# Kernel tuning notes

Hardware: AMD Instinct MI355X
Metric: run time of the kernel (lower is better)

Reference implementation:

```python
import jax, jax.numpy as jnp
import numpy as np

N_NODES, N_EDGES, HIDDEN, N_GRAPHS = 100000, 500000, 128, 2048
ATOM_DIM, BOND_DIM, OUT_DIM = 4, 3, 1


def setup_inputs() -> dict:
    key = jax.random.key(0)
    ks = jax.random.split(key, 13)
    s = 0.05  # small init scale to keep relu+scatter depth iterations numerically tame
    return {
        "x": jax.random.normal(ks[0], (N_NODES, ATOM_DIM), jnp.float32),
        "edge_index": jax.random.randint(ks[1], (2, N_EDGES), 0, N_NODES, dtype=jnp.int32),
        "edge_attr": jax.random.normal(ks[2], (N_EDGES, BOND_DIM), jnp.float32),
        "batch": jnp.sort(jax.random.randint(ks[3], (N_NODES,), 0, N_GRAPHS, dtype=jnp.int32)),
        "depth": 3,
        # DMPNN weights (bias=False)
        "W_i": jax.random.normal(ks[4], (HIDDEN, ATOM_DIM + BOND_DIM), jnp.float32) * s,
        "W_m": jax.random.normal(ks[5], (HIDDEN, HIDDEN), jnp.float32) * s,
        "W_a": jax.random.normal(ks[6], (HIDDEN, ATOM_DIM + HIDDEN), jnp.float32) * s,
        # FFN: Linear(d,4d) -> relu -> dropout(eval=identity) -> Linear(4d,d)
        "W1": jax.random.normal(ks[7], (4 * HIDDEN, HIDDEN), jnp.float32) * s,
        "b1": jnp.zeros((4 * HIDDEN,), jnp.float32),
        "W2": jax.random.normal(ks[8], (HIDDEN, 4 * HIDDEN), jnp.float32) * s,
        "b2": jnp.zeros((HIDDEN,), jnp.float32),
        "W_last": jax.random.normal(ks[9], (OUT_DIM, HIDDEN), jnp.float32) * s,
        "b_last": jnp.zeros((OUT_DIM,), jnp.float32),
    }


def reference(x, edge_index, edge_attr, batch, depth, W_i, W_m, W_a, W1, b1, W2, b2, W_last, b_last):
    src, dst = edge_index[0], edge_index[1]
    E = edge_attr.shape[0]
    N = x.shape[0]
    # h: per-edge state [E, H]
    h = jax.nn.relu(jnp.concatenate([x[src], edge_attr], axis=1) @ W_i.T)
    for _ in range(depth):
        # message: relu(W_m h) gathered at src, scatter-add to dst; PyG infers
        # dim_size from h (edge-level here), so aggregation buffer has E rows.
        m = jax.nn.relu(h @ W_m.T)
        h = h + jax.ops.segment_sum(m[src], dst, num_segments=E)
    # index_add_ edge states to nodes
    node_emb = jax.ops.segment_sum(h, dst, num_segments=N)  # [N, H]
    node_emb = jax.nn.relu(jnp.concatenate([x, node_emb], axis=1) @ W_a.T)
    # global_add_pool over graphs
    g = jax.ops.segment_sum(node_emb, batch, num_segments=N_GRAPHS)  # [G, H]
    g = jax.nn.relu(g @ W1.T + b1) @ W2.T + b2  # FFN (dropout eval = identity)
    return g @ W_last.T + b_last  # [G, OUT_DIM]
```

## Files before the change

### kernel.cpp

```cpp
#include <hip/hip_runtime.h>


#define NN 100000
#define NE 500000
#define HID 128
#define NG 2048
#define NB_SCAN 391
#define NBLKG 782

typedef __attribute__((ext_vector_type(8))) short bf16x8;
typedef __attribute__((ext_vector_type(4))) float f32x4;

__device__ __forceinline__ float b2f(ushort u) {
  return __uint_as_float(((uint)u) << 16);
}
__device__ __forceinline__ ushort f2b(float f) {
  uint u = __float_as_uint(f);
  return (ushort)((u + 0x7FFF + ((u >> 16) & 1)) >> 16);
}
__device__ __forceinline__ void acc8(float* a, bf16x8 v) {
#pragma unroll
  for (int j = 0; j < 8; ++j) a[j] += b2f((ushort)v[j]);
}
__device__ __forceinline__ bf16x8 pack8(const float* a) {
  bf16x8 o;
#pragma unroll
  for (int j = 0; j < 8; ++j) o[j] = (short)f2b(a[j]);
  return o;
}
__device__ __forceinline__ size_t taddr(int n, int c8) {
  return ((size_t)(c8 >> 4) * NN + n) * 16 + (c8 & 8);
}

__global__ __launch_bounds__(256) void k_convw(const float* __restrict__ Wm,
    const float* __restrict__ Wa, ushort* __restrict__ wmb, ushort* __restrict__ wab) {
  int i = blockIdx.x * 256 + threadIdx.x;
  if (i >= HID * HID) return;
  wmb[i] = f2b(Wm[i]);
  int c = i >> 7, k = i & 127;
  wab[i] = f2b(Wa[c * 132 + 4 + k]);
}

__global__ __launch_bounds__(256) void k_init_h(const int* __restrict__ src,
    const float* __restrict__ x, const float* __restrict__ ea,
    const float* __restrict__ Wi, ushort* __restrict__ hT) {
  __shared__ float wis[HID * 7];
  for (int i = threadIdx.x; i < HID * 7; i += 256) wis[i] = Wi[i];
  __syncthreads();
  int idx = blockIdx.x * 256 + threadIdx.x;
  int e = idx >> 7, c = idx & 127;
  if (e >= NN) return;
  int s = src[e];
  const float* w = &wis[c * 7];
  float acc = x[s*4+0]*w[0] + x[s*4+1]*w[1] + x[s*4+2]*w[2] + x[s*4+3]*w[3]
            + ea[e*3+0]*w[4] + ea[e*3+1]*w[5] + ea[e*3+2]*w[6];
  hT[((size_t)(c >> 4) * NN + e) * 16 + (c & 15)] = f2b(fmaxf(acc, 0.f));
}

__global__ __launch_bounds__(256) void k_hist2(const int* __restrict__ dst,
    int* __restrict__ cnt, int* __restrict__ cnt_lo) {
  int e = blockIdx.x * 256 + threadIdx.x;
  if (e >= NE) return;
  int d = dst[e];
  atomicAdd(&cnt[d], 1);
  if (e < NN) atomicAdd(&cnt_lo[d], 1);
}

__global__ __launch_bounds__(256) void k_scan1(const int* __restrict__ cnt,
    int* __restrict__ outp, int* __restrict__ bsums) {
  __shared__ int s[256];
  int t = threadIdx.x;
  int i = blockIdx.x * 256 + t;
  int v = (i < NN) ? cnt[i] : 0;
  s[t] = v;
  __syncthreads();
  for (int off = 1; off < 256; off <<= 1) {
    int u = (t >= off) ? s[t - off] : 0;
    __syncthreads();
    s[t] += u;
    __syncthreads();
  }
  if (i < NN) outp[i] = s[t] - v;
  if (t == 255) bsums[blockIdx.x] = s[255];
}

__global__ __launch_bounds__(512) void k_scan2(int* __restrict__ bsums) {
  __shared__ int s[512];
  int t = threadIdx.x;
  int v = (t < NB_SCAN) ? bsums[t] : 0;
  s[t] = v;
  __syncthreads();
  for (int off = 1; off < 512; off <<= 1) {
    int u = (t >= off) ? s[t - off] : 0;
    __syncthreads();
    s[t] += u;
    __syncthreads();
  }
  if (t < NB_SCAN) bsums[t] = s[t] - v;
}

__global__ __launch_bounds__(256) void k_scan3(int* __restrict__ outp,
                                               const int* __restrict__ bsums) {
  int i = blockIdx.x * 256 + threadIdx.x;
  if (i < NN) outp[i] += bsums[blockIdx.x];
  if (i == 0) outp[NN] = NE;
}

__global__ __launch_bounds__(256) void k_mid(const int* __restrict__ rowptr,
    const int* __restrict__ cnt_lo, int* __restrict__ midp) {
  int i = blockIdx.x * 256 + threadIdx.x;
  if (i < NN) midp[i] = rowptr[i] + cnt_lo[i];
}

__global__ __launch_bounds__(256) void k_fill2(const int* __restrict__ src,
    const int* __restrict__ dst, const int* __restrict__ rowptr,
    const int* __restrict__ midp, int* __restrict__ cur_lo,
    int* __restrict__ cur_hi, int* __restrict__ csr_src, int* __restrict__ csr_eid) {
  int e = blockIdx.x * 256 + threadIdx.x;
  if (e >= NE) return;
  int d = dst[e];
  int o;
  if (e < NN) o = rowptr[d] + atomicAdd(&cur_lo[d], 1);
  else        o = midp[d]   + atomicAdd(&cur_hi[d], 1);
  csr_src[o] = src[e];
  csr_eid[o] = e;
}

__global__ __launch_bounds__(256) void k_goff(const int* __restrict__ batch,
                                              int* __restrict__ goff) {
  int g = blockIdx.x * 256 + threadIdx.x;
  if (g > NG) return;
  int lo = 0, hi = NN;
  while (lo < hi) { int mid = (lo + hi) >> 1; if (batch[mid] < g) lo = mid + 1; else hi = mid; }
  goff[g] = lo;
}

template <bool HASX>
__global__ __launch_bounds__(256) void k_mfma(const ushort* __restrict__ A,
    const ushort* __restrict__ Wb, const float* __restrict__ X,
    const float* __restrict__ WaF, ushort* __restrict__ O, int nrows) {
  int tid = threadIdx.x;
  int wave = tid >> 6;
  int lane = tid & 63;
  int wr = wave >> 1, wc = wave & 1;
  int row0 = blockIdx.x * 64 + wr * 32;
  int col0 = wc * 64;
  int l15 = lane & 15, l4 = lane >> 4;

  f32x4 acc[2][4];
#pragma unroll
  for (int mi = 0; mi < 2; ++mi)
#pragma unroll
    for (int ni = 0; ni < 4; ++ni) acc[mi][ni] = (f32x4){0.f, 0.f, 0.f, 0.f};

  if (HASX) {
    float4 wv[4];
#pragma unroll
    for (int ni = 0; ni < 4; ++ni)
      wv[ni] = *reinterpret_cast<const float4*>(&WaF[(size_t)(col0 + ni * 16 + l15) * 132]);
#pragma unroll
    for (int mi = 0; mi < 2; ++mi)
#pragma unroll
      for (int j = 0; j < 4; ++j) {
        int r = row0 + mi * 16 + l4 * 4 + j;
        if (r < nrows) {
          float4 xv = *reinterpret_cast<const float4*>(&X[(size_t)r * 4]);
#pragma unroll
          for (int ni = 0; ni < 4; ++ni)
            acc[mi][ni][j] = xv.x * wv[ni].x + xv.y * wv[ni].y
                           + xv.z * wv[ni].z + xv.w * wv[ni].w;
        }
      }
  }

  const bf16x8 zero8 = {0, 0, 0, 0, 0, 0, 0, 0};
#pragma unroll
  for (int k0 = 0; k0 < HID; k0 += 32) {
    bf16x8 a[2], b[4];
    int c8 = k0 + l4 * 8;
#pragma unroll
    for (int mi = 0; mi < 2; ++mi) {
      int r = row0 + mi * 16 + l15;
      a[mi] = (r < nrows)
            ? *reinterpret_cast<const bf16x8*>(&A[taddr(r, c8)])
            : zero8;
    }
#pragma unroll
    for (int ni = 0; ni < 4; ++ni) {
      int c = col0 + ni * 16 + l15;
      b[ni] = *reinterpret_cast<const bf16x8*>(&Wb[(size_t)c * HID + k0 + l4 * 8]);
    }
#pragma unroll
    for (int mi = 0; mi < 2; ++mi)
#pragma unroll
      for (int ni = 0; ni < 4; ++ni)
        acc[mi][ni] = __builtin_amdgcn_mfma_f32_16x16x32_bf16(a[mi], b[ni], acc[mi][ni], 0, 0, 0);
  }

#pragma unroll
  for (int mi = 0; mi < 2; ++mi)
#pragma unroll
    for (int j = 0; j < 4; ++j) {
      int r = row0 + mi * 16 + l4 * 4 + j;
      if (r >= nrows) continue;
#pragma unroll
      for (int ni = 0; ni < 4; ++ni) {
        int plane = wc * 4 + ni;
        O[((size_t)plane * NN + r) * 16 + l15] = f2b(fmaxf(acc[mi][ni][j], 0.f));
      }
    }
}

__global__ __launch_bounds__(256) void k_gather_t(const ushort* __restrict__ mT,
    const int* __restrict__ rowptr, const int* __restrict__ csr_src,
    ushort* __restrict__ hT) {
  int t = blockIdx.x / NBLKG;
  int b = blockIdx.x % NBLKG;
  int p = threadIdx.x >> 1;
  int half8 = (threadIdx.x & 1) * 8;
  int n = b * 128 + p;
  if (n >= NN) return;
  size_t plane = (size_t)t * NN;
  size_t base = (plane + n) * 16 + half8;
  float a[8];
  bf16x8 hv = *reinterpret_cast<const bf16x8*>(&hT[base]);
#pragma unroll
  for (int j = 0; j < 8; ++j) a[j] = b2f((ushort)hv[j]);
  int beg = rowptr[n], end = rowptr[n + 1];
  for (int i = beg; i < end; i += 8) {
    int ss[8];
#pragma unroll
    for (int k = 0; k < 8; ++k) ss[k] = csr_src[min(i + k, end - 1)];
    bf16x8 v[8];
#pragma unroll
    for (int k = 0; k < 8; ++k)
      v[k] = *reinterpret_cast<const bf16x8*>(&mT[(plane + ss[k]) * 16 + half8]);
#pragma unroll
    for (int k = 0; k < 8; ++k)
      if (i + k < end) acc8(a, v[k]);
  }
  *reinterpret_cast<bf16x8*>(&hT[base]) = pack8(a);
}

__device__ __forceinline__ void h0acc(float* a, const float w[8][7],
                                      float4 xv, float e0, float e1, float e2) {
#pragma unroll
  for (int j = 0; j < 8; ++j) {
    float t = xv.x*w[j][0] + xv.y*w[j][1] + xv.z*w[j][2] + xv.w*w[j][3]
            + e0*w[j][4] + e1*w[j][5] + e2*w[j][6];
    a[j] += fmaxf(t, 0.f);
  }
}

__global__ __launch_bounds__(256) void k_node_agg2(const ushort* __restrict__ h,
    const int* __restrict__ rowptr, const int* __restrict__ midp,
    const int* __restrict__ csr_src, const int* __restrict__ csr_eid,
    const float* __restrict__ x, const float* __restrict__ ea,
    const float* __restrict__ Wi, ushort* __restrict__ ne) {
  int idx = blockIdx.x * 256 + threadIdx.x;
  int n = idx >> 4;
  int c8 = (idx & 15) * 8;
  float w[8][7];
#pragma unroll
  for (int j = 0; j < 8; ++j)
#pragma unroll
    for (int k = 0; k < 7; ++k) w[j][k] = Wi[(c8 + j) * 7 + k];
  if (n >= NN) return;
  int beg = rowptr[n], mid = midp[n], end = rowptr[n + 1];
  float a[8];
#pragma unroll
  for (int j = 0; j < 8; ++j) a[j] = 0.f;

  for (int i = beg; i < mid; i += 4) {
    int ee[4];
#pragma unroll
    for (int k = 0; k < 4; ++k) ee[k] = csr_eid[min(i + k, mid - 1)];
    bf16x8 v[4];
#pragma unroll
    for (int k = 0; k < 4; ++k)
      v[k] = *reinterpret_cast<const bf16x8*>(&h[taddr(ee[k], c8)]);
#pragma unroll
    for (int k = 0; k < 4; ++k)
      if (i + k < mid) acc8(a, v[k]);
  }

  for (int i = mid; i < end; i += 4) {
    int s4[4], e4[4];
#pragma unroll
    for (int k = 0; k < 4; ++k) {
      int ii = min(i + k, end - 1);
      s4[k] = csr_src[ii];
      e4[k] = csr_eid[ii];
    }
    float4 xv[4];
    float ev[4][3];
#pragma unroll
    for (int k = 0; k < 4; ++k) {
      xv[k] = *reinterpret_cast<const float4*>(&x[(size_t)s4[k] * 4]);
      ev[k][0] = ea[(size_t)e4[k]*3+0];
      ev[k][1] = ea[(size_t)e4[k]*3+1];
      ev[k][2] = ea[(size_t)e4[k]*3+2];
    }
#pragma unroll
    for (int k = 0; k < 4; ++k)
      if (i + k < end) h0acc(a, w, xv[k], ev[k][0], ev[k][1], ev[k][2]);
  }
  *reinterpret_cast<bf16x8*>(&ne[taddr(n, c8)]) = pack8(a);
}

__global__ __launch_bounds__(256) void k_pool(const ushort* __restrict__ na,
    const int* __restrict__ goff, float* __restrict__ g) {
  int idx = blockIdx.x * 256 + threadIdx.x;
  int gid = idx >> 4;
  if (gid >= NG) return;
  int c8 = (idx & 15) * 8;
  size_t pbase = (size_t)(c8 >> 4) * NN;
  int off = c8 & 8;
  int beg = goff[gid], end = goff[gid + 1];
  float a[8];
#pragma unroll
  for (int j = 0; j < 8; ++j) a[j] = 0.f;
  for (int n = beg; n < end; ++n)
    acc8(a, *reinterpret_cast<const bf16x8*>(&na[(pbase + n) * 16 + off]));
  *reinterpret_cast<float4*>(&g[(size_t)gid * HID + c8]) = make_float4(a[0], a[1], a[2], a[3]);
  *reinterpret_cast<float4*>(&g[(size_t)gid * HID + c8 + 4]) = make_float4(a[4], a[5], a[6], a[7]);
}

template <bool RELU>
__global__ __launch_bounds__(256) void k_gemm64(const float* __restrict__ A,
    const float* __restrict__ W, const float* __restrict__ bias,
    float* __restrict__ O, int nrows, int K, int N) {
  __shared__ float As[64][33];
  __shared__ float Bs[32][68];
  int tid = threadIdx.x;
  int row0 = blockIdx.x * 64;
  int col0 = blockIdx.y * 64;
  int tn = tid & 15;
  int tm = tid >> 4;
  float acc[4][4];
#pragma unroll
  for (int i = 0; i < 4; ++i)
#pragma unroll
    for (int j = 0; j < 4; ++j) acc[i][j] = 0.f;

  for (int k0 = 0; k0 < K; k0 += 32) {
    int ar = tid >> 3;
    int ak = (tid & 7) << 2;
#pragma unroll
    for (int rr = 0; rr < 2; ++rr) {
      int r = row0 + ar + rr * 32;
      float4 v = make_float4(0.f, 0.f, 0.f, 0.f);
      if (r < nrows) v = *reinterpret_cast<const float4*>(&A[(size_t)r * K + k0 + ak]);
      As[ar + rr*32][ak+0] = v.x; As[ar + rr*32][ak+1] = v.y;
      As[ar + rr*32][ak+2] = v.z; As[ar + rr*32][ak+3] = v.w;
    }
    int c = tid & 63;
    int kq = tid >> 6;
#pragma unroll
    for (int it = 0; it < 2; ++it) {
      int kk = kq * 4 + it * 16;
      float4 v = *reinterpret_cast<const float4*>(&W[(size_t)(col0 + c) * K + k0 + kk]);
      Bs[kk+0][c] = v.x; Bs[kk+1][c] = v.y; Bs[kk+2][c] = v.z; Bs[kk+3][c] = v.w;
    }
    __syncthreads();
#pragma unroll 8
    for (int k = 0; k < 32; ++k) {
      float av[4];
#pragma unroll
      for (int i = 0; i < 4; ++i) av[i] = As[tm*4 + i][k];
      float4 bv = *reinterpret_cast<const float4*>(&Bs[k][tn*4]);
#pragma unroll
      for (int i = 0; i < 4; ++i) {
        acc[i][0] = fmaf(av[i], bv.x, acc[i][0]);
        acc[i][1] = fmaf(av[i], bv.y, acc[i][1]);
        acc[i][2] = fmaf(av[i], bv.z, acc[i][2]);
        acc[i][3] = fmaf(av[i], bv.w, acc[i][3]);
      }
    }
    __syncthreads();
  }
#pragma unroll
  for (int i = 0; i < 4; ++i) {
    int r = row0 + tm * 4 + i;
    if (r >= nrows) continue;
    float4 o;
    int c = col0 + tn * 4;
    o.x = acc[i][0] + bias[c+0];
    o.y = acc[i][1] + bias[c+1];
    o.z = acc[i][2] + bias[c+2];
    o.w = acc[i][3] + bias[c+3];
    if (RELU) {
      o.x = fmaxf(o.x, 0.f); o.y = fmaxf(o.y, 0.f);
      o.z = fmaxf(o.z, 0.f); o.w = fmaxf(o.w, 0.f);
    }
    *reinterpret_cast<float4*>(&O[(size_t)r * N + c]) = o;
  }
}

__global__ __launch_bounds__(256) void k_last(const float* __restrict__ g3,
    const float* __restrict__ Wl, const float* __restrict__ bl,
    float* __restrict__ out) {
  int wid = (blockIdx.x * 256 + threadIdx.x) >> 6;
  int lane = threadIdx.x & 63;
  if (wid >= NG) return;
  float a = g3[(size_t)wid*128 + lane] * Wl[lane]
          + g3[(size_t)wid*128 + 64 + lane] * Wl[64 + lane];
  for (int off = 32; off; off >>= 1) a += __shfl_down(a, off);
  if (lane == 0) out[wid] = a + bl[0];
}

extern "C" void kernel_launch(void* const* d_in, const int* in_sizes, int n_in,
                              void* d_out, int out_size, void* d_ws, size_t ws_size,
                              hipStream_t stream) {
  const float* x    = (const float*)d_in[0];
  const int*   eidx = (const int*)d_in[1];
  const float* ea   = (const float*)d_in[2];
  const int*   batch= (const int*)d_in[3];
  const float* Wi   = (const float*)d_in[5];
  const float* Wm   = (const float*)d_in[6];
  const float* Wa   = (const float*)d_in[7];
  const float* W1   = (const float*)d_in[8];
  const float* b1   = (const float*)d_in[9];
  const float* W2   = (const float*)d_in[10];
  const float* b2   = (const float*)d_in[11];
  const float* Wl   = (const float*)d_in[12];
  const float* bl   = (const float*)d_in[13];
  float* out = (float*)d_out;

  const int* src = eidx;
  const int* dst = eidx + NE;

  char* p = (char*)d_ws;
  ushort* hb  = (ushort*)p; p += (size_t)NN * HID * 2;
  ushort* mb  = (ushort*)p; p += (size_t)NN * HID * 2;
  ushort* wmb = (ushort*)p; p += (size_t)HID * HID * 2;
  ushort* wab = (ushort*)p; p += (size_t)HID * HID * 2;
  float* g  = (float*)p; p += (size_t)NG * 128 * 4;
  float* g2 = (float*)p; p += (size_t)NG * 512 * 4;
  float* g3 = (float*)p; p += (size_t)NG * 128 * 4;
  int* csr_src = (int*)p; p += (size_t)NE * 4;
  int* csr_eid = (int*)p; p += (size_t)NE * 4;
  int* cnt    = (int*)p; p += (size_t)NN * 4;
  int* cnt_lo = (int*)p; p += (size_t)NN * 4;
  int* cur_lo = (int*)p; p += (size_t)NN * 4;
  int* cur_hi = (int*)p; p += (size_t)NN * 4;
  int* rowptr = (int*)p; p += (size_t)(NN + 4) * 4;
  int* midp   = (int*)p; p += (size_t)NN * 4;
  int* bsums  = (int*)p; p += 512 * 4;
  int* goff   = (int*)p; p += (size_t)(NG + 4) * 4;

  hipMemsetAsync(cnt, 0, (size_t)4 * NN * sizeof(int), stream);
  k_hist2<<<(NE + 255) / 256, 256, 0, stream>>>(dst, cnt, cnt_lo);
  k_scan1<<<NB_SCAN, 256, 0, stream>>>(cnt, rowptr, bsums);
  k_scan2<<<1, 512, 0, stream>>>(bsums);
  k_scan3<<<NB_SCAN, 256, 0, stream>>>(rowptr, bsums);
  k_mid  <<<NB_SCAN, 256, 0, stream>>>(rowptr, cnt_lo, midp);
  k_fill2<<<(NE + 255) / 256, 256, 0, stream>>>(src, dst, rowptr, midp,
                                                cur_lo, cur_hi, csr_src, csr_eid);
  k_goff <<<(NG + 256) / 256, 256, 0, stream>>>(batch, goff);

  k_convw<<<(HID * HID + 255) / 256, 256, 0, stream>>>(Wm, Wa, wmb, wab);

  k_init_h<<<(NN * HID) / 256, 256, 0, stream>>>(src, x, ea, Wi, hb);

  int ggrid = (NN + 63) / 64;
  for (int it = 0; it < 3; ++it) {
    k_mfma<false><<<ggrid, 256, 0, stream>>>(hb, wmb, nullptr, nullptr, mb, NN);
    k_gather_t<<<8 * NBLKG, 256, 0, stream>>>(mb, rowptr, csr_src, hb);
  }

  k_node_agg2<<<(NN * 16 + 255) / 256, 256, 0, stream>>>(hb, rowptr, midp,
                                                csr_src, csr_eid, x, ea, Wi, mb);
  k_mfma<true><<<ggrid, 256, 0, stream>>>(mb, wab, x, Wa, hb, NN);

  k_pool<<<(NG * 16 + 255) / 256, 256, 0, stream>>>(hb, goff, g);

  dim3 grid1((NG + 63) / 64, 512 / 64);
  k_gemm64<true><<<grid1, 256, 0, stream>>>(g, W1, b1, g2, NG, 128, 512);
  dim3 grid2((NG + 63) / 64, 128 / 64);
  k_gemm64<false><<<grid2, 256, 0, stream>>>(g2, W2, b2, g3, NG, 512, 128);
  k_last<<<(NG * 64) / 256, 256, 0, stream>>>(g3, Wl, bl, out);
}
```

Baseline: 494.1 us.

## Prepack edge features in CSR order and interleave gather blocks across planes

The CSR fill kernel now also writes a packed bf16 record of x[src] and edge_attr for each high edge, in CSR order. The node aggregation then reads one contiguous 16-byte record per edge instead of gathering x and edge_attr indirectly. Block indices for gather and node aggregation are interleaved so that consecutive blocks cover different feature planes of the same node range. Node aggregation now uses plane-major indexing, and the init kernel computes 8 channels per thread with a vector store. This adds a bf16 rounding of the input features for the recomputed h0 terms and a new 8 MB workspace buffer.

Measured after the change: 439.7 us. 11.0% less time.

```diff
diff --git a/kernel.cpp b/kernel.cpp
--- a/kernel.cpp
+++ b/kernel.cpp
@@ -6,7 +6,7 @@
 #define HID 128
 #define NG 2048
 #define NB_SCAN 391
-#define NBLKG 782
+#define NBLK128 782
 
 typedef __attribute__((ext_vector_type(8))) short bf16x8;
 typedef __attribute__((ext_vector_type(4))) float f32x4;
@@ -41,20 +41,28 @@
   wab[i] = f2b(Wa[c * 132 + 4 + k]);
 }
 
-__global__ __launch_bounds__(256) void k_init_h(const int* __restrict__ src,
+__global__ __launch_bounds__(256) void k_init_h8(const int* __restrict__ src,
     const float* __restrict__ x, const float* __restrict__ ea,
     const float* __restrict__ Wi, ushort* __restrict__ hT) {
   __shared__ float wis[HID * 7];
   for (int i = threadIdx.x; i < HID * 7; i += 256) wis[i] = Wi[i];
   __syncthreads();
   int idx = blockIdx.x * 256 + threadIdx.x;
-  int e = idx >> 7, c = idx & 127;
+  int e = idx >> 4, chunk = idx & 15;
   if (e >= NN) return;
   int s = src[e];
-  const float* w = &wis[c * 7];
-  float acc = x[s*4+0]*w[0] + x[s*4+1]*w[1] + x[s*4+2]*w[2] + x[s*4+3]*w[3]
-            + ea[e*3+0]*w[4] + ea[e*3+1]*w[5] + ea[e*3+2]*w[6];
-  hT[((size_t)(c >> 4) * NN + e) * 16 + (c & 15)] = f2b(fmaxf(acc, 0.f));
+  float4 xv = *reinterpret_cast<const float4*>(&x[(size_t)s * 4]);
+  float e0 = ea[(size_t)e*3+0], e1 = ea[(size_t)e*3+1], e2 = ea[(size_t)e*3+2];
+  const float* w = &wis[chunk * 56];
+  float a[8];
+#pragma unroll
+  for (int j = 0; j < 8; ++j) {
+    const float* wj = &w[j * 7];
+    float t = xv.x*wj[0] + xv.y*wj[1] + xv.z*wj[2] + xv.w*wj[3]
+            + e0*wj[4] + e1*wj[5] + e2*wj[6];
+    a[j] = fmaxf(t, 0.f);
+  }
+  *reinterpret_cast<bf16x8*>(&hT[((size_t)(chunk >> 1) * NN + e) * 16 + (chunk & 1) * 8]) = pack8(a);
 }
 
 __global__ __launch_bounds__(256) void k_hist2(const int* __restrict__ dst,
@@ -112,17 +120,32 @@
   if (i < NN) midp[i] = rowptr[i] + cnt_lo[i];
 }
 
-__global__ __launch_bounds__(256) void k_fill2(const int* __restrict__ src,
+__global__ __launch_bounds__(256) void k_fill2z(const int* __restrict__ src,
     const int* __restrict__ dst, const int* __restrict__ rowptr,
     const int* __restrict__ midp, int* __restrict__ cur_lo,
-    int* __restrict__ cur_hi, int* __restrict__ csr_src, int* __restrict__ csr_eid) {
+    int* __restrict__ cur_hi, int* __restrict__ csr_src, int* __restrict__ csr_eid,
+    const float* __restrict__ x, const float* __restrict__ ea,
+    ushort* __restrict__ zpk) {
   int e = blockIdx.x * 256 + threadIdx.x;
   if (e >= NE) return;
   int d = dst[e];
+  int s = src[e];
   int o;
-  if (e < NN) o = rowptr[d] + atomicAdd(&cur_lo[d], 1);
-  else        o = midp[d]   + atomicAdd(&cur_hi[d], 1);
-  csr_src[o] = src[e];
+  if (e < NN) {
+    o = rowptr[d] + atomicAdd(&cur_lo[d], 1);
+  } else {
+    o = midp[d] + atomicAdd(&cur_hi[d], 1);
+    float4 xv = *reinterpret_cast<const float4*>(&x[(size_t)s * 4]);
+    bf16x8 z;
+    z[0] = (short)f2b(xv.x); z[1] = (short)f2b(xv.y);
+    z[2] = (short)f2b(xv.z); z[3] = (short)f2b(xv.w);
+    z[4] = (short)f2b(ea[(size_t)e*3+0]);
+    z[5] = (short)f2b(ea[(size_t)e*3+1]);
+    z[6] = (short)f2b(ea[(size_t)e*3+2]);
+    z[7] = 0;
+    *reinterpret_cast<bf16x8*>(&zpk[(size_t)o * 8]) = z;
+  }
+  csr_src[o] = s;
   csr_eid[o] = e;
 }
 
@@ -211,17 +234,16 @@
     }
 }
 
-__global__ __launch_bounds__(256) void k_gather_t(const ushort* __restrict__ mT,
+__global__ __launch_bounds__(256) void k_gather_x(const ushort* __restrict__ mT,
     const int* __restrict__ rowptr, const int* __restrict__ csr_src,
     ushort* __restrict__ hT) {
-  int t = blockIdx.x / NBLKG;
-  int b = blockIdx.x % NBLKG;
-  int p = threadIdx.x >> 1;
+  int plane = blockIdx.x & 7;
+  int nb = blockIdx.x >> 3;
+  int n = nb * 128 + (threadIdx.x >> 1);
+  if (n >= NN) return;
   int half8 = (threadIdx.x & 1) * 8;
-  int n = b * 128 + p;
-  if (n >= NN) return;
-  size_t plane = (size_t)t * NN;
-  size_t base = (plane + n) * 16 + half8;
+  size_t pb = (size_t)plane * NN;
+  size_t base = (pb + n) * 16 + half8;
   float a[8];
   bf16x8 hv = *reinterpret_cast<const bf16x8*>(&hT[base]);
 #pragma unroll
@@ -234,7 +256,7 @@
     bf16x8 v[8];
 #pragma unroll
     for (int k = 0; k < 8; ++k)
-      v[k] = *reinterpret_cast<const bf16x8*>(&mT[(plane + ss[k]) * 16 + half8]);
+      v[k] = *reinterpret_cast<const bf16x8*>(&mT[(pb + ss[k]) * 16 + half8]);
 #pragma unroll
     for (int k = 0; k < 8; ++k)
       if (i + k < end) acc8(a, v[k]);
@@ -242,30 +264,22 @@
   *reinterpret_cast<bf16x8*>(&hT[base]) = pack8(a);
 }
 
-__device__ __forceinline__ void h0acc(float* a, const float w[8][7],
-                                      float4 xv, float e0, float e1, float e2) {
-#pragma unroll
-  for (int j = 0; j < 8; ++j) {
-    float t = xv.x*w[j][0] + xv.y*w[j][1] + xv.z*w[j][2] + xv.w*w[j][3]
-            + e0*w[j][4] + e1*w[j][5] + e2*w[j][6];
-    a[j] += fmaxf(t, 0.f);
-  }
-}
-
-__global__ __launch_bounds__(256) void k_node_agg2(const ushort* __restrict__ h,
+__global__ __launch_bounds__(256) void k_node_agg_x(const ushort* __restrict__ hT,
     const int* __restrict__ rowptr, const int* __restrict__ midp,
-    const int* __restrict__ csr_src, const int* __restrict__ csr_eid,
-    const float* __restrict__ x, const float* __restrict__ ea,
-    const float* __restrict__ Wi, ushort* __restrict__ ne) {
-  int idx = blockIdx.x * 256 + threadIdx.x;
-  int n = idx >> 4;
-  int c8 = (idx & 15) * 8;
+    const int* __restrict__ csr_eid, const ushort* __restrict__ zpk,
+    const float* __restrict__ Wi, ushort* __restrict__ neT) {
+  int plane = blockIdx.x & 7;
+  int nb = blockIdx.x >> 3;
+  int n = nb * 128 + (threadIdx.x >> 1);
+  if (n >= NN) return;
+  int half8 = (threadIdx.x & 1) * 8;
+  int c8 = plane * 16 + half8;
   float w[8][7];
 #pragma unroll
   for (int j = 0; j < 8; ++j)
 #pragma unroll
     for (int k = 0; k < 7; ++k) w[j][k] = Wi[(c8 + j) * 7 + k];
-  if (n >= NN) return;
+  size_t pb = (size_t)plane * NN;
   int beg = rowptr[n], mid = midp[n], end = rowptr[n + 1];
   float a[8];
 #pragma unroll
@@ -278,34 +292,33 @@
     bf16x8 v[4];
 #pragma unroll
     for (int k = 0; k < 4; ++k)
-      v[k] = *reinterpret_cast<const bf16x8*>(&h[taddr(ee[k], c8)]);
+      v[k] = *reinterpret_cast<const bf16x8*>(&hT[(pb + ee[k]) * 16 + half8]);
 #pragma unroll
     for (int k = 0; k < 4; ++k)
       if (i + k < mid) acc8(a, v[k]);
   }
 
   for (int i = mid; i < end; i += 4) {
-    int s4[4], e4[4];
+    bf16x8 zv[4];
+#pragma unroll
+    for (int k = 0; k < 4; ++k)
+      zv[k] = *reinterpret_cast<const bf16x8*>(&zpk[(size_t)min(i + k, end - 1) * 8]);
 #pragma unroll
     for (int k = 0; k < 4; ++k) {
-      int ii = min(i + k, end - 1);
-      s4[k] = csr_src[ii];
-      e4[k] = csr_eid[ii];
-    }
-    float4 xv[4];
-    float ev[4][3];
-#pragma unroll
-    for (int k = 0; k < 4; ++k) {
-      xv[k] = *reinterpret_cast<const float4*>(&x[(size_t)s4[k] * 4]);
-      ev[k][0] = ea[(size_t)e4[k]*3+0];
-      ev[k][1] = ea[(size_t)e4[k]*3+1];
-      ev[k][2] = ea[(size_t)e4[k]*3+2];
-    }
-#pragma unroll
-    for (int k = 0; k < 4; ++k)
-      if (i + k < end) h0acc(a, w, xv[k], ev[k][0], ev[k][1], ev[k][2]);
-  }
-  *reinterpret_cast<bf16x8*>(&ne[taddr(n, c8)]) = pack8(a);
+      if (i + k >= end) break;
+      float z0 = b2f((ushort)zv[k][0]), z1 = b2f((ushort)zv[k][1]);
+      float z2 = b2f((ushort)zv[k][2]), z3 = b2f((ushort)zv[k][3]);
+      float z4 = b2f((ushort)zv[k][4]), z5 = b2f((ushort)zv[k][5]);
+      float z6 = b2f((ushort)zv[k][6]);
+#pragma unroll
+      for (int j = 0; j < 8; ++j) {
+        float t = z0*w[j][0] + z1*w[j][1] + z2*w[j][2] + z3*w[j][3]
+                + z4*w[j][4] + z5*w[j][5] + z6*w[j][6];
+        a[j] += fmaxf(t, 0.f);
+      }
+    }
+  }
+  *reinterpret_cast<bf16x8*>(&neT[(pb + n) * 16 + half8]) = pack8(a);
 }
 
 __global__ __launch_bounds__(256) void k_pool(const ushort* __restrict__ na,
@@ -435,6 +448,7 @@
   ushort* mb  = (ushort*)p; p += (size_t)NN * HID * 2;
   ushort* wmb = (ushort*)p; p += (size_t)HID * HID * 2;
   ushort* wab = (ushort*)p; p += (size_t)HID * HID * 2;
+  ushort* zpk = (ushort*)p; p += (size_t)NE * 8 * 2;
   float* g  = (float*)p; p += (size_t)NG * 128 * 4;
   float* g2 = (float*)p; p += (size_t)NG * 512 * 4;
   float* g3 = (float*)p; p += (size_t)NG * 128 * 4;
@@ -455,22 +469,23 @@
   k_scan2<<<1, 512, 0, stream>>>(bsums);
   k_scan3<<<NB_SCAN, 256, 0, stream>>>(rowptr, bsums);
   k_mid  <<<NB_SCAN, 256, 0, stream>>>(rowptr, cnt_lo, midp);
-  k_fill2<<<(NE + 255) / 256, 256, 0, stream>>>(src, dst, rowptr, midp,
-                                                cur_lo, cur_hi, csr_src, csr_eid);
+  k_fill2z<<<(NE + 255) / 256, 256, 0, stream>>>(src, dst, rowptr, midp,
+                                                 cur_lo, cur_hi, csr_src, csr_eid,
+                                                 x, ea, zpk);
   k_goff <<<(NG + 256) / 256, 256, 0, stream>>>(batch, goff);
 
   k_convw<<<(HID * HID + 255) / 256, 256, 0, stream>>>(Wm, Wa, wmb, wab);
 
-  k_init_h<<<(NN * HID) / 256, 256, 0, stream>>>(src, x, ea, Wi, hb);
+  k_init_h8<<<(NN * 16 + 255) / 256, 256, 0, stream>>>(src, x, ea, Wi, hb);
 
   int ggrid = (NN + 63) / 64;
   for (int it = 0; it < 3; ++it) {
     k_mfma<false><<<ggrid, 256, 0, stream>>>(hb, wmb, nullptr, nullptr, mb, NN);
-    k_gather_t<<<8 * NBLKG, 256, 0, stream>>>(mb, rowptr, csr_src, hb);
-  }
-
-  k_node_agg2<<<(NN * 16 + 255) / 256, 256, 0, stream>>>(hb, rowptr, midp,
-                                                csr_src, csr_eid, x, ea, Wi, mb);
+    k_gather_x<<<8 * NBLK128, 256, 0, stream>>>(mb, rowptr, csr_src, hb);
+  }
+
+  k_node_agg_x<<<8 * NBLK128, 256, 0, stream>>>(hb, rowptr, midp, csr_eid,
+                                                zpk, Wi, mb);
   k_mfma<true><<<ggrid, 256, 0, stream>>>(mb, wab, x, Wa, hb, NN);
 
   k_pool<<<(NG * 16 + 255) / 256, 256, 0, stream>>>(hb, goff, g);
```
